# Kernel optimization log

Hardware: AMD Instinct MI355X
Metric: run time of the kernel (lower is better)

Reference implementation:

```python
import jax, jax.numpy as jnp
import numpy as np

NUM_TILES = 64
TPC = 8            # tiles per cluster
GRID = 16          # spline grid size
EPS = 1e-5


def setup_inputs() -> dict:
    key = jax.random.key(0)
    ks = jax.random.split(key, 6)
    B, S, D, T, DH, G = 2, 1024, 512, NUM_TILES, 128, GRID
    x = jax.random.normal(ks[0], (B, S, D), dtype=jnp.float32)
    gamma = jnp.ones((D,), jnp.float32)
    beta = jnp.zeros((D,), jnp.float32)
    # torch layouts: down.weight [DH, D], up.weight [D, DH]
    Wd = jax.random.normal(ks[1], (T, DH, D), dtype=jnp.float32) * 0.02
    spline_bases = jax.random.normal(ks[2], (T, DH, G), dtype=jnp.float32) * 0.1
    spline_slopes = jax.random.normal(ks[3], (T, DH, G), dtype=jnp.float32) * 0.1
    Wu = jax.random.normal(ks[4], (T, D, DH), dtype=jnp.float32) * 0.02
    scale = jnp.full((T,), 0.1, jnp.float32)
    return {"x": x, "gamma": gamma, "beta": beta, "Wd": Wd,
            "spline_bases": spline_bases, "spline_slopes": spline_slopes,
            "Wu": Wu, "scale": scale}


def reference(x, gamma, beta, Wd, spline_bases, spline_slopes, Wu, scale):
    B, S, D = x.shape
    T, DH, _ = Wd.shape
    C = T // TPC
    N = B * S

    # LayerNorm
    mu = x.mean(-1, keepdims=True)
    var = ((x - mu) ** 2).mean(-1, keepdims=True)
    xn = (x - mu) * jax.lax.rsqrt(var + EPS) * gamma + beta
    xf = xn.reshape(N, D)

    # Signatures (first call: ema == current tile signatures)
    tile_sigs = jnp.sign(Wd.mean(axis=1))                         # [T, D]
    cluster_sigs = jnp.sign(tile_sigs.reshape(C, TPC, D).mean(1))  # [C, D]

    # Hierarchical routing: cluster -> tile
    in_sigs = jnp.sign(xf)                                        # [N, D]
    best_c = jnp.argmax(in_sigs @ cluster_sigs.T, axis=-1)        # [N]
    tile_scores = (in_sigs @ tile_sigs.T).reshape(N, C, TPC)      # [N, C, TPC]
    sc = jnp.take_along_axis(tile_scores, best_c[:, None, None], axis=1)[:, 0, :]
    local_best = jnp.argmax(sc, axis=-1)                          # [N]
    tidx = best_c * TPC + local_best                              # [N]

    # Dispatch: gather per-token expert weights, down-project
    h = jnp.einsum('nd,nhd->nh', xf, Wd[tidx])                    # [N, DH]

    # Spline nonlinearity
    hn = jax.nn.sigmoid(h)
    idx = jnp.clip((hn * GRID).astype(jnp.int32), 0, GRID - 1)    # [N, DH]
    base = jnp.take_along_axis(spline_bases[tidx], idx[..., None], axis=-1)[..., 0]
    slope = jnp.take_along_axis(spline_slopes[tidx], idx[..., None], axis=-1)[..., 0]
    local_pos = hn * GRID - idx.astype(h.dtype)                   # (hn - idx*cell)/cell
    hs = base + slope * local_pos                                 # [N, DH]

    # Up-project, per-tile scale, combine (dropout is identity in eval)
    y = jnp.einsum('nh,ndh->nd', hs, Wu[tidx]) * scale[tidx][:, None]
    return x + y.reshape(B, S, D)
```

## Files before the change

kernel.cpp:

```cpp
#include <hip/hip_runtime.h>
#include <hip/hip_bf16.h>
#include <math.h>

#define NTILES 64
#define TPC 8
#define NCLUST 8
#define GRID_SZ 16
#define DIM 512
#define DHID 128
#define NTOK 2048
#define LN_EPS 1e-5f
#define TB 16
#define NCHUNK_MAX 192

typedef __attribute__((ext_vector_type(8))) short bf16x8;
typedef __attribute__((ext_vector_type(4))) float f32x4;
typedef unsigned long long u64;

static __device__ __forceinline__ unsigned short bf16bits(float f) {
    union { __hip_bfloat16 h; unsigned short s; } u;
    u.h = __float2bfloat16(f);
    return u.s;
}

static __device__ __forceinline__ bf16x8 cvt8(const float* p) {
    float4 a = *(const float4*)p;
    float4 b = *(const float4*)(p + 4);
    float e[8] = {a.x, a.y, a.z, a.w, b.x, b.y, b.z, b.w};
    bf16x8 v;
    #pragma unroll
    for (int i = 0; i < 8; ++i) v[i] = (short)bf16bits(e[i]);
    return v;
}

static __device__ __forceinline__ bool route_chunk(const int* counts, int lane, int cb,
                                                   int& t, int& base, int& m) {
    int cnt_l = counts[lane];
    int nck = (cnt_l + TB - 1) / TB;
    int pre = nck;
    #pragma unroll
    for (int off = 1; off < 64; off <<= 1) {
        int u = __shfl_up(pre, off);
        if (lane >= off) pre += u;
    }
    int total = __shfl(pre, 63);
    pre -= nck;
    if (cb >= total) return false;
    u64 msk = __ballot(cb >= pre && cb < pre + nck);
    t = (int)__builtin_ctzll(msk);
    base = (cb - __shfl(pre, t)) * TB;
    m = min(TB, __shfl(cnt_l, t) - base);
    return true;
}

__global__ __launch_bounds__(256) void k_prep(const float* __restrict__ x,
                                              const float* __restrict__ gamma,
                                              const float* __restrict__ beta,
                                              const float* __restrict__ Wd,
                                              float* __restrict__ psum,
                                              unsigned short* __restrict__ wd_b,
                                              unsigned short* __restrict__ xn_b,
                                              int* __restrict__ counts) {
    int bid = blockIdx.x;
    int tid = threadIdx.x;
    if (bid < 512) {
        int t = bid >> 3, part = bid & 7;
        const float* basep = Wd + ((size_t)t * DHID + part * 16) * DIM;
        unsigned short* bb = wd_b + ((size_t)t * DHID + part * 16) * DIM;
        #pragma unroll
        for (int k2 = 0; k2 < 2; ++k2) {
            int d = tid + k2 * 256;
            float s = 0.f;
            #pragma unroll
            for (int j = 0; j < 16; ++j) {
                float v = basep[(size_t)j * DIM + d];
                s += v;
                bb[(size_t)j * DIM + d] = bf16bits(v);
            }
            psum[((size_t)t * 8 + part) * DIM + d] = s;
        }
        if (bid == 0 && tid < NTILES) counts[tid] = 0;
    } else {
        int n = (bid - 512) * 4 + (tid >> 6);
        int lane = tid & 63;
        const float* xr = x + (size_t)n * DIM;
        float v[8];
        float sum = 0.f;
        #pragma unroll
        for (int j = 0; j < 8; ++j) { float t = xr[lane + 64 * j]; v[j] = t; sum += t; }
        #pragma unroll
        for (int off = 32; off; off >>= 1) sum += __shfl_xor(sum, off);
        float mu = sum * (1.f / DIM);
        float sq = 0.f;
        #pragma unroll
        for (int j = 0; j < 8; ++j) { float t = v[j] - mu; sq += t * t; }
        #pragma unroll
        for (int off = 32; off; off >>= 1) sq += __shfl_xor(sq, off);
        float rs = rsqrtf(sq * (1.f / DIM) + LN_EPS);
        #pragma unroll
        for (int j = 0; j < 8; ++j) {
            int d = lane + 64 * j;
            float xv = (v[j] - mu) * rs * gamma[d] + beta[d];
            xn_b[(size_t)n * DIM + d] = bf16bits(xv);
        }
    }
}

__global__ __launch_bounds__(512) void k_csig(const float* __restrict__ psum,
                                              u64* __restrict__ tbits,
                                              u64* __restrict__ cbits,
                                              u64* __restrict__ cmask) {
    int c = blockIdx.x;
    int w = threadIdx.x >> 6;
    int lane = threadIdx.x & 63;
    int t = c * TPC + w;
    __shared__ u64 tb_lds[TPC][8];
    #pragma unroll
    for (int j = 0; j < 8; ++j) {
        int d = lane + 64 * j;
        float s = 0.f;
        #pragma unroll
        for (int p = 0; p < 8; ++p) s += psum[((size_t)t * 8 + p) * DIM + d];
        u64 b = __ballot(s < 0.f);
        if (lane == 0) { tbits[t * 8 + j] = b; tb_lds[w][j] = b; }
    }
    __syncthreads();
    int cnt = 0;
    #pragma unroll
    for (int k = 0; k < TPC; ++k) cnt += (int)((tb_lds[k][w] >> lane) & 1ULL);
    u64 cb = __ballot(cnt > 4);
    u64 cm = __ballot(cnt != 4);
    if (lane == 0) { cbits[c * 8 + w] = cb; cmask[c * 8 + w] = cm; }
}

__global__ __launch_bounds__(256) void k_route(const unsigned short* __restrict__ xn_b,
                                               const u64* __restrict__ tbits,
                                               const u64* __restrict__ cbits,
                                               const u64* __restrict__ cmask,
                                               int* __restrict__ counts,
                                               int* __restrict__ list) {
    int n = blockIdx.x * 4 + (threadIdx.x >> 6);
    int lane = threadIdx.x & 63;
    u64 xb[8];
    #pragma unroll
    for (int j = 0; j < 8; ++j) {
        unsigned short u = xn_b[(size_t)n * DIM + lane + 64 * j];
        xb[j] = __ballot((u & 0x8000u) != 0 && (u & 0x7fffu) != 0);
    }
    const u64* tb = tbits + lane * 8;
    int ts = 0;
    #pragma unroll
    for (int j = 0; j < 8; ++j) ts += __popcll(xb[j] ^ tb[j]);
    int tscore = DIM - 2 * ts;
    int cscore = -(1 << 30);
    if (lane < NCLUST) {
        const u64* cb = cbits + lane * 8;
        const u64* cm = cmask + lane * 8;
        int s = 0;
        #pragma unroll
        for (int j = 0; j < 8; ++j)
            s += __popcll(cm[j]) - 2 * __popcll((xb[j] ^ cb[j]) & cm[j]);
        cscore = s;
    }
    int bc = 0, best = __shfl(cscore, 0);
    #pragma unroll
    for (int k = 1; k < NCLUST; ++k) {
        int v = __shfl(cscore, k);
        if (v > best) { best = v; bc = k; }
    }
    int bt = bc * TPC, bts = __shfl(tscore, bc * TPC);
    #pragma unroll
    for (int k = 1; k < TPC; ++k) {
        int v = __shfl(tscore, bc * TPC + k);
        if (v > bts) { bts = v; bt = bc * TPC + k; }
    }
    if (lane == 0) {
        int slot = atomicAdd(&counts[bt], 1);
        list[(size_t)bt * NTOK + slot] = n;
    }
}

__global__ __launch_bounds__(512, 2) void k_ffn(const float* __restrict__ x,
                                                const unsigned short* __restrict__ xn_b,
                                                const unsigned short* __restrict__ wd_b,
                                                const float* __restrict__ sb,
                                                const float* __restrict__ ss,
                                                const float* __restrict__ Wu,
                                                const float* __restrict__ scale,
                                                const int* __restrict__ counts,
                                                const int* __restrict__ list,
                                                float* __restrict__ out) {
    int tid = threadIdx.x;
    int lane = tid & 63;
    int wv = tid >> 6;
    int cb = ((int)blockIdx.x & 7) * (NCHUNK_MAX / 8) + ((int)blockIdx.x >> 3);
    int t, base, m;
    if (!route_chunk(counts, lane, cb, t, base, m)) return;

    __shared__ __align__(16) unsigned short hsl[TB * DHID];

    int mrow = lane & 15;
    int ko = (lane >> 4) * 8;
    int tokm = list[(size_t)t * NTOK + base + min(mrow, m - 1)];

    const unsigned short* xr = xn_b + (size_t)tokm * DIM;
    const unsigned short* wr = wd_b + ((size_t)t * DHID + wv * 16 + mrow) * DIM;
    f32x4 acc0 = {0.f, 0.f, 0.f, 0.f}, acc1 = acc0;
    #pragma unroll
    for (int kk = 0; kk < 8; ++kk) {
        int d0 = kk * 32 + ko;
        int d1 = (kk + 8) * 32 + ko;
        bf16x8 a0 = *(const bf16x8*)(xr + d0);
        bf16x8 b0 = *(const bf16x8*)(wr + d0);
        acc0 = __builtin_amdgcn_mfma_f32_16x16x32_bf16(a0, b0, acc0, 0, 0, 0);
        bf16x8 a1 = *(const bf16x8*)(xr + d1);
        bf16x8 b1 = *(const bf16x8*)(wr + d1);
        acc1 = __builtin_amdgcn_mfma_f32_16x16x32_bf16(a1, b1, acc1, 0, 0, 0);
    }
    f32x4 acc = acc0 + acc1;
    int dh = wv * 16 + mrow;
    const float* sbt = sb + ((size_t)t * DHID + dh) * GRID_SZ;
    const float* sst = ss + ((size_t)t * DHID + dh) * GRID_SZ;
    #pragma unroll
    for (int r = 0; r < 4; ++r) {
        int tr = (lane >> 4) * 4 + r;
        float h = acc[r];
        float hn = 1.f / (1.f + expf(-h));
        float g = hn * (float)GRID_SZ;
        int idx = (int)g;
        idx = idx > GRID_SZ - 1 ? GRID_SZ - 1 : idx;
        float lp = g - (float)idx;
        float val = sbt[idx] + sst[idx] * lp;
        hsl[(tr * DHID + dh) ^ ((tr & 7) << 3)] = bf16bits(val);
    }
    __syncthreads();

    float sc_t = scale[t];
    bf16x8 a2[4];
    #pragma unroll
    for (int kk = 0; kk < 4; ++kk)
        a2[kk] = *(const bf16x8*)&hsl[(mrow * DHID + kk * 32 + ko) ^ ((mrow & 7) << 3)];
    #pragma unroll
    for (int nt = 0; nt < 4; ++nt) {
        int d = wv * 64 + nt * 16 + mrow;
        const float* wru = Wu + ((size_t)t * DIM + d) * DHID;
        f32x4 au = {0.f, 0.f, 0.f, 0.f};
        #pragma unroll
        for (int kk = 0; kk < 4; ++kk) {
            bf16x8 b = cvt8(wru + kk * 32 + ko);
            au = __builtin_amdgcn_mfma_f32_16x16x32_bf16(a2[kk], b, au, 0, 0, 0);
        }
        #pragma unroll
        for (int r = 0; r < 4; ++r) {
            int tr = (lane >> 4) * 4 + r;
            int tok_tr = __shfl(tokm, tr);
            if (tr < m) {
                size_t o = (size_t)tok_tr * DIM + d;
                out[o] = x[o] + au[r] * sc_t;
            }
        }
    }
}

extern "C" void kernel_launch(void* const* d_in, const int* in_sizes, int n_in,
                              void* d_out, int out_size, void* d_ws, size_t ws_size,
                              hipStream_t stream) {
    const float* x     = (const float*)d_in[0];
    const float* gamma = (const float*)d_in[1];
    const float* beta  = (const float*)d_in[2];
    const float* Wd    = (const float*)d_in[3];
    const float* sb    = (const float*)d_in[4];
    const float* ss    = (const float*)d_in[5];
    const float* Wu    = (const float*)d_in[6];
    const float* scale = (const float*)d_in[7];
    float* out = (float*)d_out;

    float* psum          = (float*)d_ws;
    u64*   tbits         = (u64*)(psum + (size_t)NTILES * 8 * DIM);
    u64*   cbits         = tbits + NTILES * 8;
    u64*   cmask         = cbits + NCLUST * 8;
    int*   counts        = (int*)(cmask + NCLUST * 8);
    int*   list          = counts + NTILES;
    unsigned short* xn_b = (unsigned short*)(list + (size_t)NTILES * NTOK);
    unsigned short* wd_b = xn_b + (size_t)NTOK * DIM;

    k_prep<<<1024, 256, 0, stream>>>(x, gamma, beta, Wd, psum, wd_b, xn_b, counts);
    k_csig<<<NCLUST, 512, 0, stream>>>(psum, tbits, cbits, cmask);
    k_route<<<NTOK / 4, 256, 0, stream>>>(xn_b, tbits, cbits, cmask, counts, list);
    k_ffn<<<NCHUNK_MAX, 512, 0, stream>>>(x, xn_b, wd_b, sb, ss, Wu, scale, counts, list, out);
}
```

Before: 51.38 us.

## Fuse tile signature reduction into prep and compute cluster majority in routing

Each tile's Wd column sums are now computed by a single 512-thread block that also writes the bf16 copy and the sign bitmask directly, so the psum buffer and the separate cluster-signature kernel go away. The routing kernel derives the cluster majority bits with a bit-sliced adder over the 8 tile bitmasks and reduces the scores with shuffles. The FFN kernel also prefetches the first Wu slice before the spline stage to hide its load latency. This saves one launch and the psum round-trip, but the Wd conversion now runs on only 64 blocks, each looping serially over 128 rows, which may reduce parallelism.

```diff
diff --git a/kernel.cpp b/kernel.cpp
--- a/kernel.cpp
+++ b/kernel.cpp
@@ -23,14 +23,20 @@
     return u.s;
 }
 
-static __device__ __forceinline__ bf16x8 cvt8(const float* p) {
-    float4 a = *(const float4*)p;
-    float4 b = *(const float4*)(p + 4);
+static __device__ __forceinline__ bf16x8 cvt8v(float4 a, float4 b) {
     float e[8] = {a.x, a.y, a.z, a.w, b.x, b.y, b.z, b.w};
     bf16x8 v;
     #pragma unroll
     for (int i = 0; i < 8; ++i) v[i] = (short)bf16bits(e[i]);
     return v;
+}
+
+static __device__ __forceinline__ bf16x8 cvt8(const float* p) {
+    return cvt8v(*(const float4*)p, *(const float4*)(p + 4));
+}
+
+static __device__ __forceinline__ u64 maj3(u64 a, u64 b, u64 c) {
+    return (a & b) | (c & (a ^ b));
 }
 
 static __device__ __forceinline__ bool route_chunk(const int* counts, int lane, int cb,
@@ -53,36 +59,41 @@
     return true;
 }
 
-__global__ __launch_bounds__(256) void k_prep(const float* __restrict__ x,
+__global__ __launch_bounds__(512) void k_prep(const float* __restrict__ x,
                                               const float* __restrict__ gamma,
                                               const float* __restrict__ beta,
                                               const float* __restrict__ Wd,
-                                              float* __restrict__ psum,
                                               unsigned short* __restrict__ wd_b,
                                               unsigned short* __restrict__ xn_b,
+                                              u64* __restrict__ tbits,
                                               int* __restrict__ counts) {
     int bid = blockIdx.x;
     int tid = threadIdx.x;
-    if (bid < 512) {
-        int t = bid >> 3, part = bid & 7;
-        const float* basep = Wd + ((size_t)t * DHID + part * 16) * DIM;
-        unsigned short* bb = wd_b + ((size_t)t * DHID + part * 16) * DIM;
-        #pragma unroll
-        for (int k2 = 0; k2 < 2; ++k2) {
-            int d = tid + k2 * 256;
-            float s = 0.f;
-            #pragma unroll
-            for (int j = 0; j < 16; ++j) {
-                float v = basep[(size_t)j * DIM + d];
-                s += v;
-                bb[(size_t)j * DIM + d] = bf16bits(v);
-            }
-            psum[((size_t)t * 8 + part) * DIM + d] = s;
-        }
+    int lane = tid & 63;
+    int wv = tid >> 6;
+    if (bid < NTILES) {
+        int t = bid;
         if (bid == 0 && tid < NTILES) counts[tid] = 0;
+        const float* bp = Wd + (size_t)t * DHID * DIM + tid;
+        unsigned short* bb = wd_b + (size_t)t * DHID * DIM + tid;
+        float s0 = 0.f, s1 = 0.f, s2 = 0.f, s3 = 0.f;
+        #pragma unroll 4
+        for (int j = 0; j < DHID; j += 4) {
+            float v0 = bp[(size_t)(j + 0) * DIM];
+            float v1 = bp[(size_t)(j + 1) * DIM];
+            float v2 = bp[(size_t)(j + 2) * DIM];
+            float v3 = bp[(size_t)(j + 3) * DIM];
+            bb[(size_t)(j + 0) * DIM] = bf16bits(v0);
+            bb[(size_t)(j + 1) * DIM] = bf16bits(v1);
+            bb[(size_t)(j + 2) * DIM] = bf16bits(v2);
+            bb[(size_t)(j + 3) * DIM] = bf16bits(v3);
+            s0 += v0; s1 += v1; s2 += v2; s3 += v3;
+        }
+        float s = (s0 + s1) + (s2 + s3);
+        u64 b = __ballot(s < 0.f);
+        if (lane == 0) tbits[t * 8 + wv] = b;
     } else {
-        int n = (bid - 512) * 4 + (tid >> 6);
-        int lane = tid & 63;
+        int n = (bid - NTILES) * 8 + wv;
         const float* xr = x + (size_t)n * DIM;
         float v[8];
         float sum = 0.f;
@@ -106,37 +117,8 @@
     }
 }
 
-__global__ __launch_bounds__(512) void k_csig(const float* __restrict__ psum,
-                                              u64* __restrict__ tbits,
-                                              u64* __restrict__ cbits,
-                                              u64* __restrict__ cmask) {
-    int c = blockIdx.x;
-    int w = threadIdx.x >> 6;
-    int lane = threadIdx.x & 63;
-    int t = c * TPC + w;
-    __shared__ u64 tb_lds[TPC][8];
-    #pragma unroll
-    for (int j = 0; j < 8; ++j) {
-        int d = lane + 64 * j;
-        float s = 0.f;
-        #pragma unroll
-        for (int p = 0; p < 8; ++p) s += psum[((size_t)t * 8 + p) * DIM + d];
-        u64 b = __ballot(s < 0.f);
-        if (lane == 0) { tbits[t * 8 + j] = b; tb_lds[w][j] = b; }
-    }
-    __syncthreads();
-    int cnt = 0;
-    #pragma unroll
-    for (int k = 0; k < TPC; ++k) cnt += (int)((tb_lds[k][w] >> lane) & 1ULL);
-    u64 cb = __ballot(cnt > 4);
-    u64 cm = __ballot(cnt != 4);
-    if (lane == 0) { cbits[c * 8 + w] = cb; cmask[c * 8 + w] = cm; }
-}
-
 __global__ __launch_bounds__(256) void k_route(const unsigned short* __restrict__ xn_b,
                                                const u64* __restrict__ tbits,
-                                               const u64* __restrict__ cbits,
-                                               const u64* __restrict__ cmask,
                                                int* __restrict__ counts,
                                                int* __restrict__ list) {
     int n = blockIdx.x * 4 + (threadIdx.x >> 6);
@@ -152,20 +134,32 @@
     #pragma unroll
     for (int j = 0; j < 8; ++j) ts += __popcll(xb[j] ^ tb[j]);
     int tscore = DIM - 2 * ts;
-    int cscore = -(1 << 30);
-    if (lane < NCLUST) {
-        const u64* cb = cbits + lane * 8;
-        const u64* cm = cmask + lane * 8;
-        int s = 0;
-        #pragma unroll
-        for (int j = 0; j < 8; ++j)
-            s += __popcll(cm[j]) - 2 * __popcll((xb[j] ^ cb[j]) & cm[j]);
-        cscore = s;
-    }
-    int bc = 0, best = __shfl(cscore, 0);
+
+    int c = lane >> 3, jw = lane & 7;
+    u64 x0 = tbits[(c * TPC + 0) * 8 + jw], x1 = tbits[(c * TPC + 1) * 8 + jw];
+    u64 x2 = tbits[(c * TPC + 2) * 8 + jw], x3 = tbits[(c * TPC + 3) * 8 + jw];
+    u64 x4 = tbits[(c * TPC + 4) * 8 + jw], x5 = tbits[(c * TPC + 5) * 8 + jw];
+    u64 x6 = tbits[(c * TPC + 6) * 8 + jw], x7 = tbits[(c * TPC + 7) * 8 + jw];
+    u64 s0 = x0 ^ x1 ^ x2, c0 = maj3(x0, x1, x2);
+    u64 s1 = x3 ^ x4 ^ x5, c1 = maj3(x3, x4, x5);
+    u64 s2 = x6 ^ x7,      c2 = x6 & x7;
+    u64 t0 = s0 ^ s1 ^ s2, t1 = maj3(s0, s1, s2);
+    u64 p = c0 ^ c1, q = c0 & c1;
+    u64 r = c2 ^ t1, s_ = c2 & t1;
+    u64 S0 = p ^ r, car = p & r;
+    u64 W0 = (q ^ s_) ^ car;
+    u64 W1 = (q & s_) | (car & (q ^ s_));
+    u64 cbit = W1 | (W0 & (S0 | t0));
+    u64 cmsk = ~(W0 & ~W1 & ~S0 & ~t0);
+    int ps = __popcll(cmsk) - 2 * __popcll((xb[jw] ^ cbit) & cmsk);
+    ps += __shfl_xor(ps, 1);
+    ps += __shfl_xor(ps, 2);
+    ps += __shfl_xor(ps, 4);
+
+    int bc = 0, best = __shfl(ps, 0);
     #pragma unroll
     for (int k = 1; k < NCLUST; ++k) {
-        int v = __shfl(cscore, k);
+        int v = __shfl(ps, k * 8);
         if (v > best) { best = v; bc = k; }
     }
     int bt = bc * TPC, bts = __shfl(tscore, bc * TPC);
@@ -218,6 +212,15 @@
         acc1 = __builtin_amdgcn_mfma_f32_16x16x32_bf16(a1, b1, acc1, 0, 0, 0);
     }
     f32x4 acc = acc0 + acc1;
+
+    const float* wru0 = Wu + ((size_t)t * DIM + wv * 64 + mrow) * DHID;
+    float4 pfa[4], pfb[4];
+    #pragma unroll
+    for (int kk = 0; kk < 4; ++kk) {
+        pfa[kk] = *(const float4*)(wru0 + kk * 32 + ko);
+        pfb[kk] = *(const float4*)(wru0 + kk * 32 + ko + 4);
+    }
+
     int dh = wv * 16 + mrow;
     const float* sbt = sb + ((size_t)t * DHID + dh) * GRID_SZ;
     const float* sst = ss + ((size_t)t * DHID + dh) * GRID_SZ;
@@ -247,7 +250,8 @@
         f32x4 au = {0.f, 0.f, 0.f, 0.f};
         #pragma unroll
         for (int kk = 0; kk < 4; ++kk) {
-            bf16x8 b = cvt8(wru + kk * 32 + ko);
+            bf16x8 b = (nt == 0) ? cvt8v(pfa[kk], pfb[kk])
+                                 : cvt8(wru + kk * 32 + ko);
             au = __builtin_amdgcn_mfma_f32_16x16x32_bf16(a2[kk], b, au, 0, 0, 0);
         }
         #pragma unroll
@@ -275,17 +279,13 @@
     const float* scale = (const float*)d_in[7];
     float* out = (float*)d_out;
 
-    float* psum          = (float*)d_ws;
-    u64*   tbits         = (u64*)(psum + (size_t)NTILES * 8 * DIM);
-    u64*   cbits         = tbits + NTILES * 8;
-    u64*   cmask         = cbits + NCLUST * 8;
-    int*   counts        = (int*)(cmask + NCLUST * 8);
+    u64*   tbits         = (u64*)d_ws;
+    int*   counts        = (int*)(tbits + NTILES * 8);
     int*   list          = counts + NTILES;
     unsigned short* xn_b = (unsigned short*)(list + (size_t)NTILES * NTOK);
     unsigned short* wd_b = xn_b + (size_t)NTOK * DIM;
 
-    k_prep<<<1024, 256, 0, stream>>>(x, gamma, beta, Wd, psum, wd_b, xn_b, counts);
-    k_csig<<<NCLUST, 512, 0, stream>>>(psum, tbits, cbits, cmask);
-    k_route<<<NTOK / 4, 256, 0, stream>>>(xn_b, tbits, cbits, cmask, counts, list);
+    k_prep<<<NTILES + NTOK / 8, 512, 0, stream>>>(x, gamma, beta, Wd, wd_b, xn_b, tbits, counts);
+    k_route<<<NTOK / 4, 256, 0, stream>>>(xn_b, tbits, counts, list);
     k_ffn<<<NCHUNK_MAX, 512, 0, stream>>>(x, xn_b, wd_b, sb, ss, Wu, scale, counts, list, out);
 }
```

Result: no change. 50.49 us (-1.7%).
